# Kernel tuning notes

Measured on AMD Instinct MI355X. Metric: run time of the kernel, lower is better.

Reference implementation:

```python
import jax, jax.numpy as jnp
import numpy as np


def setup_inputs() -> dict:
    key = jax.random.key(0)
    k1, k2, k3 = jax.random.split(key, 3)
    B, S, D_IN, D_OUT = 4, 2048, 4096, 4096
    x = jax.random.normal(k1, (B, S, D_IN), dtype=jnp.float32)
    # int8 quantized weight, stored as int8 (values in [-127, 127])
    weight = jax.random.randint(k2, (D_OUT, D_IN), -127, 128, dtype=jnp.int8)
    weight_scaler = jax.random.uniform(k3, (D_OUT,), dtype=jnp.float32) * 0.02
    return {"x": x, "weight": weight, "weight_scaler": weight_scaler}


def reference(x, weight, weight_scaler):
    # quant path: dequantize weight with per-output-channel scale, then F.linear
    w = weight.astype(jnp.float32) * weight_scaler[:, None]  # [D_OUT, D_IN]
    # F.linear(x, w) == x @ w.T
    return jnp.einsum('bsd,od->bso', x, w)
```

## Files before the change

### kernel.cpp

```cpp
#include <hip/hip_runtime.h>
#include <cstdint>
#include <cstddef>

typedef int i32x4 __attribute__((ext_vector_type(4)));

static __device__ __forceinline__ int pack4(float4 v, float inv) {
  int a = __float2int_rn(v.x * inv) & 0xFF;
  int b = __float2int_rn(v.y * inv) & 0xFF;
  int c = __float2int_rn(v.z * inv) & 0xFF;
  int d = __float2int_rn(v.w * inv) & 0xFF;
  return a | (b << 8) | (c << 16) | (d << 24);
}

__global__ __launch_bounds__(256) void prep_kernel(
    const float* __restrict__ x, signed char* __restrict__ xq, float* __restrict__ xs,
    const int* __restrict__ w, signed char* __restrict__ wq,
    int K, int xrows) {
  const int t = threadIdx.x;
  if ((int)blockIdx.x < xrows) {
    const int row = blockIdx.x;
    const float4* xr = (const float4*)(x + (size_t)row * K);
    const int n4 = K >> 2;
    __shared__ float wmax[4];
    if (n4 == 1024) {
      float4 v0 = xr[t], v1 = xr[t + 256], v2 = xr[t + 512], v3 = xr[t + 768];
      float amax = fmaxf(fmaxf(fabsf(v0.x), fabsf(v0.y)),
                         fmaxf(fabsf(v0.z), fabsf(v0.w)));
      amax = fmaxf(amax, fmaxf(fmaxf(fabsf(v1.x), fabsf(v1.y)),
                               fmaxf(fabsf(v1.z), fabsf(v1.w))));
      amax = fmaxf(amax, fmaxf(fmaxf(fabsf(v2.x), fabsf(v2.y)),
                               fmaxf(fabsf(v2.z), fabsf(v2.w))));
      amax = fmaxf(amax, fmaxf(fmaxf(fabsf(v3.x), fabsf(v3.y)),
                               fmaxf(fabsf(v3.z), fabsf(v3.w))));
#pragma unroll
      for (int off = 32; off > 0; off >>= 1)
        amax = fmaxf(amax, __shfl_xor(amax, off, 64));
      if ((t & 63) == 0) wmax[t >> 6] = amax;
      __syncthreads();
      amax = fmaxf(fmaxf(wmax[0], wmax[1]), fmaxf(wmax[2], wmax[3]));
      const float inv = (amax > 0.f) ? 127.f / amax : 0.f;
      if (t == 0) xs[row] = amax / 127.f;
      int* o = (int*)(xq + (size_t)row * K);
      o[t]       = pack4(v0, inv);
      o[t + 256] = pack4(v1, inv);
      o[t + 512] = pack4(v2, inv);
      o[t + 768] = pack4(v3, inv);
    } else {
      float amax = 0.f;
      for (int i = t; i < n4; i += 256) {
        float4 v = xr[i];
        amax = fmaxf(amax, fmaxf(fmaxf(fabsf(v.x), fabsf(v.y)),
                                 fmaxf(fabsf(v.z), fabsf(v.w))));
      }
#pragma unroll
      for (int off = 32; off > 0; off >>= 1)
        amax = fmaxf(amax, __shfl_xor(amax, off, 64));
      if ((t & 63) == 0) wmax[t >> 6] = amax;
      __syncthreads();
      amax = fmaxf(fmaxf(wmax[0], wmax[1]), fmaxf(wmax[2], wmax[3]));
      const float inv = (amax > 0.f) ? 127.f / amax : 0.f;
      if (t == 0) xs[row] = amax / 127.f;
      int* o = (int*)(xq + (size_t)row * K);
      for (int i = t; i < n4; i += 256) {
        float4 v = xr[i];
        o[i] = pack4(v, inv);
      }
    }
  } else {
    const size_t g = (size_t)(blockIdx.x - xrows) * 256 + t;
    int4 v = ((const int4*)w)[g];
    ((int*)wq)[g] = (v.x & 0xFF) | ((v.y & 0xFF) << 8) |
                    ((v.z & 0xFF) << 16) | ((v.w & 0xFF) << 24);
  }
}

static __device__ __forceinline__ void gld_lds16(const void* g, void* l) {
  __builtin_amdgcn_global_load_lds(
      (const __attribute__((address_space(1))) unsigned int*)g,
      (__attribute__((address_space(3))) unsigned int*)l,
      16, 0, 0);
}

__global__ __launch_bounds__(512, 2) void gemm_i8_2ph(
    const signed char* __restrict__ A,
    const signed char* __restrict__ B,
    const float* __restrict__ xs,
    const float* __restrict__ ws,
    float* __restrict__ C,
    int M, int N, int K) {
  __shared__ __align__(16) signed char lds[131072];

  const int tid  = threadIdx.x;
  const int lane = tid & 63;
  const int wave = tid >> 6;
  const int wm   = wave >> 2;
  const int wn   = wave & 3;
  const int q    = lane >> 4;
  const int r16  = lane & 15;
  const int e    = lane & 7;

  const unsigned nwg = gridDim.x * gridDim.y;
  unsigned id = blockIdx.y * gridDim.x + blockIdx.x;
  if ((nwg & 7u) == 0u) id = (id & 7u) * (nwg >> 3) + (id >> 3);
  const int m0 = (int)(id / gridDim.x) << 8;
  const int n0 = (int)(id % gridDim.x) << 8;

  const int NT = K >> 7;

  const int srow   = tid >> 3;
  const int schunk = ((tid & 7) ^ (srow & 7)) << 4;
  const signed char* sA = A + (size_t)(m0 + srow) * K + schunk;
  const signed char* sB = B + (size_t)(n0 + srow) * K + schunk;
  signed char* lW = lds + wave * 1024;

  const int aro = ((wm << 4) + r16) << 7;
  const int bro = r16 << 7;
  const int cs  = (q ^ e) << 4;

  i32x4 acc[8][4];
#pragma unroll
  for (int i = 0; i < 8; ++i)
#pragma unroll
    for (int j = 0; j < 4; ++j) acc[i][j] = (i32x4){0, 0, 0, 0};
  i32x4 af[4][2], bf[2][2][2];

#define STAGE(Tv, Gv)                                                        \
  do {                                                                       \
    const int t_ = (Tv);                                                     \
    if (t_ < NT) {                                                           \
      const int mat_ = (Gv) & 1, half_ = (Gv) >> 1;                          \
      signed char* l_ = lW + ((t_ & 1) << 15) + (mat_ << 16) + (half_ << 14);\
      const signed char* g_ = (mat_ ? sB : sA) +                             \
                              (size_t)(half_ << 7) * K + ((size_t)t_ << 7);  \
      gld_lds16(g_, l_);                                                     \
      gld_lds16(g_ + (size_t)64 * K, l_ + 8192);                             \
    }                                                                        \
  } while (0)

#define READ_A(MH)                                                           \
  _Pragma("unroll") for (int i_ = 0; i_ < 4; ++i_)                           \
    _Pragma("unroll") for (int kh_ = 0; kh_ < 2; ++kh_)                      \
      af[i_][kh_] = *(const i32x4*)(pA + ((((MH) << 2) + i_) << 12) + aro +  \
                                    (cs ^ (kh_ << 6)));

#define READ_B                                                               \
  _Pragma("unroll") for (int nh_ = 0; nh_ < 2; ++nh_)                        \
    _Pragma("unroll") for (int j_ = 0; j_ < 2; ++j_)                         \
      _Pragma("unroll") for (int kh_ = 0; kh_ < 2; ++kh_)                    \
        bf[nh_][j_][kh_] = *(const i32x4*)(pB + (nh_ << 14) + (wn << 12) +   \
                                           (j_ << 11) + bro + (cs ^ (kh_ << 6)));

#define MFMA_HALF(MH)                                                        \
  __builtin_amdgcn_s_setprio(1);                                             \
  _Pragma("unroll") for (int kh_ = 0; kh_ < 2; ++kh_)                        \
    _Pragma("unroll") for (int i_ = 0; i_ < 4; ++i_)                         \
      _Pragma("unroll") for (int nh_ = 0; nh_ < 2; ++nh_)                    \
        _Pragma("unroll") for (int j_ = 0; j_ < 2; ++j_)                     \
          acc[((MH) << 2) + i_][(nh_ << 1) + j_] =                           \
              __builtin_amdgcn_mfma_i32_16x16x64_i8(                         \
                  af[i_][kh_], bf[nh_][j_][kh_],                             \
                  acc[((MH) << 2) + i_][(nh_ << 1) + j_], 0, 0, 0);          \
  __builtin_amdgcn_s_setprio(0);

  STAGE(0, 0); STAGE(0, 1); STAGE(0, 2); STAGE(0, 3);
  STAGE(1, 0); STAGE(1, 1);
  asm volatile("s_waitcnt vmcnt(4)" ::: "memory");
  __builtin_amdgcn_s_barrier();

  for (int t = 0; t < NT; ++t) {
    const signed char* pA = lds + ((t & 1) << 15);
    const signed char* pB = lds + 65536 + ((t & 1) << 15);
    READ_A(0);
    READ_B;
    STAGE(t + 1, 2); STAGE(t + 1, 3);
    __builtin_amdgcn_s_barrier();
    asm volatile("s_waitcnt lgkmcnt(0)" ::: "memory");
    MFMA_HALF(0);
    __builtin_amdgcn_s_barrier();
    READ_A(1);
    STAGE(t + 2, 0); STAGE(t + 2, 1);
    __builtin_amdgcn_s_barrier();
    asm volatile("s_waitcnt lgkmcnt(0)" ::: "memory");
    MFMA_HALF(1);
    if (t < NT - 2) asm volatile("s_waitcnt vmcnt(4)" ::: "memory");
    else            asm volatile("s_waitcnt vmcnt(0)" ::: "memory");
    __builtin_amdgcn_s_barrier();
  }
#undef MFMA_HALF
#undef READ_B
#undef READ_A
#undef STAGE

#pragma unroll
  for (int mt = 0; mt < 8; ++mt) {
    const int row0 = m0 + (mt << 5) + (wm << 4) + (q << 2);
    float xv[4];
#pragma unroll
    for (int r = 0; r < 4; ++r) xv[r] = xs[row0 + r];
#pragma unroll
    for (int nt = 0; nt < 4; ++nt) {
      const int col = n0 + ((nt >> 1) << 7) + (wn << 5) + ((nt & 1) << 4) + r16;
      const float s = ws[col];
      float* Cp = C + (size_t)row0 * N + col;
#pragma unroll
      for (int r = 0; r < 4; ++r)
        Cp[(size_t)r * N] = (float)acc[mt][nt][r] * xv[r] * s;
    }
  }
}

__global__ void naive_kernel(const float* __restrict__ x, const int* __restrict__ w,
                             const float* __restrict__ sc, float* __restrict__ out,
                             int M, int N, int K) {
  int idx = blockIdx.x * 256 + threadIdx.x;
  if (idx >= M * N) return;
  int m = idx / N, n = idx % N;
  const float* xr = x + (size_t)m * K;
  const int*   wr = w + (size_t)n * K;
  float acc = 0.f;
  for (int k = 0; k < K; ++k) acc += xr[k] * (float)wr[k];
  out[idx] = acc * sc[n];
}

extern "C" void kernel_launch(void* const* d_in, const int* in_sizes, int n_in,
                              void* d_out, int out_size, void* d_ws, size_t ws_size,
                              hipStream_t stream) {
  const float* x  = (const float*)d_in[0];
  const int*   w  = (const int*)d_in[1];
  const float* sc = (const float*)d_in[2];
  float* out = (float*)d_out;

  const int N = in_sizes[2];
  const int K = in_sizes[1] / N;
  const int M = in_sizes[0] / K;

  const size_t need = (size_t)M * K + (size_t)N * K + (size_t)M * 4 + 16;
  if (ws_size < need || (M & 255) || (N & 255) || (K & 127) || K < 256 ||
      (((size_t)N * K) % 1024)) {
    int total = M * N;
    naive_kernel<<<(total + 255) / 256, 256, 0, stream>>>(x, w, sc, out, M, N, K);
    return;
  }

  signed char* xq = (signed char*)d_ws;
  signed char* wq = xq + (size_t)M * K;
  float*       xsc = (float*)(wq + (size_t)N * K);

  const int wblocks = (int)(((size_t)N * K) / 1024);
  prep_kernel<<<M + wblocks, 256, 0, stream>>>(x, xq, xsc, w, wq, K, M);

  dim3 grid(N >> 8, M >> 8);
  gemm_i8_2ph<<<grid, 512, 0, stream>>>(xq, wq, xsc, sc, out, M, N, K);
}
```

Baseline: 383.6 us.

## Add wave-per-row prep kernel and reschedule GEMM main loop with fewer barriers

Adds a specialized prep kernel for K=4096 in which each wave quantizes one activation row, with no LDS reduction or block sync, and each thread packs four weight vectors. The GEMM main loop is restructured to issue global-to-LDS stages earlier, split B fragment reads per N-half, and interleave LDS reads with MFMA groups. This drops from four barriers to two per K-tile. The aim is better overlap of LDS reads and global loads with MFMA work, but correctness now depends on the sched_barrier and waitcnt ordering against buffer reuse.

```diff
diff --git a/kernel.cpp b/kernel.cpp
--- a/kernel.cpp
+++ b/kernel.cpp
@@ -10,6 +10,44 @@
   int c = __float2int_rn(v.z * inv) & 0xFF;
   int d = __float2int_rn(v.w * inv) & 0xFF;
   return a | (b << 8) | (c << 16) | (d << 24);
+}
+
+__global__ __launch_bounds__(256) void prep_fast(
+    const float* __restrict__ x, signed char* __restrict__ xq, float* __restrict__ xs,
+    const int* __restrict__ w, signed char* __restrict__ wq,
+    int xblocks) {
+  const int t = threadIdx.x;
+  if ((int)blockIdx.x < xblocks) {
+    const int lane = t & 63;
+    const int row  = ((int)blockIdx.x << 2) + (t >> 6);
+    const float4* xr = (const float4*)(x + ((size_t)row << 12));
+    float4 v[16];
+#pragma unroll
+    for (int i = 0; i < 16; ++i) v[i] = xr[(i << 6) + lane];
+    float amax = 0.f;
+#pragma unroll
+    for (int i = 0; i < 16; ++i)
+      amax = fmaxf(amax, fmaxf(fmaxf(fabsf(v[i].x), fabsf(v[i].y)),
+                               fmaxf(fabsf(v[i].z), fabsf(v[i].w))));
+#pragma unroll
+    for (int off = 32; off > 0; off >>= 1)
+      amax = fmaxf(amax, __shfl_xor(amax, off, 64));
+    const float inv = (amax > 0.f) ? 127.f / amax : 0.f;
+    if (lane == 0) xs[row] = amax / 127.f;
+    int* o = (int*)(xq + ((size_t)row << 12));
+#pragma unroll
+    for (int i = 0; i < 16; ++i) o[(i << 6) + lane] = pack4(v[i], inv);
+  } else {
+    const size_t base = (((size_t)blockIdx.x - xblocks) << 10) + t;
+    const int4* wp = (const int4*)w;
+    int* op = (int*)wq;
+#pragma unroll
+    for (int i = 0; i < 4; ++i) {
+      int4 vv = wp[base + (i << 8)];
+      op[base + (i << 8)] = (vv.x & 0xFF) | ((vv.y & 0xFF) << 8) |
+                            ((vv.z & 0xFF) << 16) | ((vv.w & 0xFF) << 24);
+    }
+  }
 }
 
 __global__ __launch_bounds__(256) void prep_kernel(
@@ -22,49 +60,24 @@
     const float4* xr = (const float4*)(x + (size_t)row * K);
     const int n4 = K >> 2;
     __shared__ float wmax[4];
-    if (n4 == 1024) {
-      float4 v0 = xr[t], v1 = xr[t + 256], v2 = xr[t + 512], v3 = xr[t + 768];
-      float amax = fmaxf(fmaxf(fabsf(v0.x), fabsf(v0.y)),
-                         fmaxf(fabsf(v0.z), fabsf(v0.w)));
-      amax = fmaxf(amax, fmaxf(fmaxf(fabsf(v1.x), fabsf(v1.y)),
-                               fmaxf(fabsf(v1.z), fabsf(v1.w))));
-      amax = fmaxf(amax, fmaxf(fmaxf(fabsf(v2.x), fabsf(v2.y)),
-                               fmaxf(fabsf(v2.z), fabsf(v2.w))));
-      amax = fmaxf(amax, fmaxf(fmaxf(fabsf(v3.x), fabsf(v3.y)),
-                               fmaxf(fabsf(v3.z), fabsf(v3.w))));
-#pragma unroll
-      for (int off = 32; off > 0; off >>= 1)
-        amax = fmaxf(amax, __shfl_xor(amax, off, 64));
-      if ((t & 63) == 0) wmax[t >> 6] = amax;
-      __syncthreads();
-      amax = fmaxf(fmaxf(wmax[0], wmax[1]), fmaxf(wmax[2], wmax[3]));
-      const float inv = (amax > 0.f) ? 127.f / amax : 0.f;
-      if (t == 0) xs[row] = amax / 127.f;
-      int* o = (int*)(xq + (size_t)row * K);
-      o[t]       = pack4(v0, inv);
-      o[t + 256] = pack4(v1, inv);
-      o[t + 512] = pack4(v2, inv);
-      o[t + 768] = pack4(v3, inv);
-    } else {
-      float amax = 0.f;
-      for (int i = t; i < n4; i += 256) {
-        float4 v = xr[i];
-        amax = fmaxf(amax, fmaxf(fmaxf(fabsf(v.x), fabsf(v.y)),
-                                 fmaxf(fabsf(v.z), fabsf(v.w))));
-      }
-#pragma unroll
-      for (int off = 32; off > 0; off >>= 1)
-        amax = fmaxf(amax, __shfl_xor(amax, off, 64));
-      if ((t & 63) == 0) wmax[t >> 6] = amax;
-      __syncthreads();
-      amax = fmaxf(fmaxf(wmax[0], wmax[1]), fmaxf(wmax[2], wmax[3]));
-      const float inv = (amax > 0.f) ? 127.f / amax : 0.f;
-      if (t == 0) xs[row] = amax / 127.f;
-      int* o = (int*)(xq + (size_t)row * K);
-      for (int i = t; i < n4; i += 256) {
-        float4 v = xr[i];
-        o[i] = pack4(v, inv);
-      }
+    float amax = 0.f;
+    for (int i = t; i < n4; i += 256) {
+      float4 v = xr[i];
+      amax = fmaxf(amax, fmaxf(fmaxf(fabsf(v.x), fabsf(v.y)),
+                               fmaxf(fabsf(v.z), fabsf(v.w))));
+    }
+#pragma unroll
+    for (int off = 32; off > 0; off >>= 1)
+      amax = fmaxf(amax, __shfl_xor(amax, off, 64));
+    if ((t & 63) == 0) wmax[t >> 6] = amax;
+    __syncthreads();
+    amax = fmaxf(fmaxf(wmax[0], wmax[1]), fmaxf(wmax[2], wmax[3]));
+    const float inv = (amax > 0.f) ? 127.f / amax : 0.f;
+    if (t == 0) xs[row] = amax / 127.f;
+    int* o = (int*)(xq + (size_t)row * K);
+    for (int i = t; i < n4; i += 256) {
+      float4 v = xr[i];
+      o[i] = pack4(v, inv);
     }
   } else {
     const size_t g = (size_t)(blockIdx.x - xrows) * 256 + t;
@@ -81,7 +94,7 @@
       16, 0, 0);
 }
 
-__global__ __launch_bounds__(512, 2) void gemm_i8_2ph(
+__global__ __launch_bounds__(512, 2) void gemm_i8_pipe(
     const signed char* __restrict__ A,
     const signed char* __restrict__ B,
     const float* __restrict__ xs,
@@ -143,23 +156,21 @@
       af[i_][kh_] = *(const i32x4*)(pA + ((((MH) << 2) + i_) << 12) + aro +  \
                                     (cs ^ (kh_ << 6)));
 
-#define READ_B                                                               \
-  _Pragma("unroll") for (int nh_ = 0; nh_ < 2; ++nh_)                        \
-    _Pragma("unroll") for (int j_ = 0; j_ < 2; ++j_)                         \
-      _Pragma("unroll") for (int kh_ = 0; kh_ < 2; ++kh_)                    \
-        bf[nh_][j_][kh_] = *(const i32x4*)(pB + (nh_ << 14) + (wn << 12) +   \
-                                           (j_ << 11) + bro + (cs ^ (kh_ << 6)));
-
-#define MFMA_HALF(MH)                                                        \
+#define READ_B(NH)                                                           \
+  _Pragma("unroll") for (int j_ = 0; j_ < 2; ++j_)                           \
+    _Pragma("unroll") for (int kh_ = 0; kh_ < 2; ++kh_)                      \
+      bf[NH][j_][kh_] = *(const i32x4*)(pB + ((NH) << 14) + (wn << 12) +     \
+                                        (j_ << 11) + bro + (cs ^ (kh_ << 6)));
+
+#define MFMA_NH(MH, NH)                                                      \
   __builtin_amdgcn_s_setprio(1);                                             \
   _Pragma("unroll") for (int kh_ = 0; kh_ < 2; ++kh_)                        \
     _Pragma("unroll") for (int i_ = 0; i_ < 4; ++i_)                         \
-      _Pragma("unroll") for (int nh_ = 0; nh_ < 2; ++nh_)                    \
-        _Pragma("unroll") for (int j_ = 0; j_ < 2; ++j_)                     \
-          acc[((MH) << 2) + i_][(nh_ << 1) + j_] =                           \
-              __builtin_amdgcn_mfma_i32_16x16x64_i8(                         \
-                  af[i_][kh_], bf[nh_][j_][kh_],                             \
-                  acc[((MH) << 2) + i_][(nh_ << 1) + j_], 0, 0, 0);          \
+      _Pragma("unroll") for (int j_ = 0; j_ < 2; ++j_)                       \
+        acc[((MH) << 2) + i_][((NH) << 1) + j_] =                            \
+            __builtin_amdgcn_mfma_i32_16x16x64_i8(                           \
+                af[i_][kh_], bf[(NH)][j_][kh_],                              \
+                acc[((MH) << 2) + i_][((NH) << 1) + j_], 0, 0, 0);           \
   __builtin_amdgcn_s_setprio(0);
 
   STAGE(0, 0); STAGE(0, 1); STAGE(0, 2); STAGE(0, 3);
@@ -170,23 +181,25 @@
   for (int t = 0; t < NT; ++t) {
     const signed char* pA = lds + ((t & 1) << 15);
     const signed char* pB = lds + 65536 + ((t & 1) << 15);
+    STAGE(t + 1, 2); STAGE(t + 1, 3);
     READ_A(0);
-    READ_B;
-    STAGE(t + 1, 2); STAGE(t + 1, 3);
+    READ_B(0);
+    asm volatile("s_waitcnt lgkmcnt(0)" ::: "memory");
+    __builtin_amdgcn_sched_barrier(0);
     __builtin_amdgcn_s_barrier();
-    asm volatile("s_waitcnt lgkmcnt(0)" ::: "memory");
-    MFMA_HALF(0);
-    __builtin_amdgcn_s_barrier();
+    STAGE(t + 2, 0); STAGE(t + 2, 1);
+    READ_B(1);
+    MFMA_NH(0, 0);
+    MFMA_NH(0, 1);
     READ_A(1);
-    STAGE(t + 2, 0); STAGE(t + 2, 1);
-    __builtin_amdgcn_s_barrier();
-    asm volatile("s_waitcnt lgkmcnt(0)" ::: "memory");
-    MFMA_HALF(1);
+    MFMA_NH(1, 0);
+    MFMA_NH(1, 1);
     if (t < NT - 2) asm volatile("s_waitcnt vmcnt(4)" ::: "memory");
     else            asm volatile("s_waitcnt vmcnt(0)" ::: "memory");
+    __builtin_amdgcn_sched_barrier(0);
     __builtin_amdgcn_s_barrier();
   }
-#undef MFMA_HALF
+#undef MFMA_NH
 #undef READ_B
 #undef READ_A
 #undef STAGE
@@ -246,9 +259,15 @@
   signed char* wq = xq + (size_t)M * K;
   float*       xsc = (float*)(wq + (size_t)N * K);
 
-  const int wblocks = (int)(((size_t)N * K) / 1024);
-  prep_kernel<<<M + wblocks, 256, 0, stream>>>(x, xq, xsc, w, wq, K, M);
+  if (K == 4096 && (M & 3) == 0 && (((size_t)N * K) % 4096) == 0) {
+    const int xblocks = M >> 2;
+    const int wblocks = (int)(((size_t)N * K) >> 12);
+    prep_fast<<<xblocks + wblocks, 256, 0, stream>>>(x, xq, xsc, w, wq, xblocks);
+  } else {
+    const int wblocks = (int)(((size_t)N * K) / 1024);
+    prep_kernel<<<M + wblocks, 256, 0, stream>>>(x, xq, xsc, w, wq, K, M);
+  }
 
   dim3 grid(N >> 8, M >> 8);
-  gemm_i8_2ph<<<grid, 512, 0, stream>>>(xq, wq, xsc, sc, out, M, N, K);
-}
+  gemm_i8_pipe<<<grid, 512, 0, stream>>>(xq, wq, xsc, sc, out, M, N, K);
+}
```

After: 384.8 us. No clear change (+0.3%).
